# Kernel optimization log

Hardware: AMD Instinct MI355X
Metric: run time of the kernel (lower is better)

The kernel has to match this reference:

```python
import jax, jax.numpy as jnp
import numpy as np

PATCH = 14   # vision_config.patch_size
MERGE = 2    # spatial_merge_size
D = 1024     # vision_config.hidden_size
# pixel (H, W) per image; all dims divisible by PATCH*MERGE = 28
IMAGE_SIZES = np.array([[1540, 1232], [1120, 1540], [896, 1260],
                        [1540, 1540], [1260, 896], [728, 1540]], dtype=np.int64)


def setup_inputs() -> dict:
    key = jax.random.key(0)
    k1, k2 = jax.random.split(key)
    hs = IMAGE_SIZES[:, 0] // PATCH
    ws = IMAGE_SIZES[:, 1] // PATCH
    total_tokens = int(np.sum(hs * ws))  # 47820
    image_features = jax.random.normal(k1, (total_tokens, D), dtype=jnp.float32)
    # nn.Linear(D*MERGE**2 -> D, bias=False): weight [D, D*MERGE**2]
    weight = jax.random.normal(k2, (D, D * MERGE * MERGE), dtype=jnp.float32) * 0.02
    return {"image_features": image_features, "weight": weight,
            "image_sizes": IMAGE_SIZES}


def _merge_patches(image_features, image_sizes):
    """Per-image unfold(kernel=stride=MERGE) -> [n_blocks, D*MERGE^2], concatenated."""
    m = MERGE
    d = image_features.shape[-1]
    sizes = np.asarray(image_sizes)
    hs = sizes[:, 0] // PATCH
    ws = sizes[:, 1] // PATCH
    offsets = np.concatenate([[0], np.cumsum(hs * ws)])
    grids = []
    for i in range(sizes.shape[0]):
        h, w = int(hs[i]), int(ws[i])
        x = jax.lax.dynamic_slice_in_dim(image_features, int(offsets[i]), h * w, 0)
        # [h, w, d] -> blocks of m x m; torch unfold layout is (d, kh, kw) channel-major
        x = x.reshape(h // m, m, w // m, m, d)
        x = x.transpose(0, 2, 4, 1, 3)           # [h/m, w/m, d, m, m]
        x = x.reshape((h // m) * (w // m), d * m * m)
        grids.append(x)
    return jnp.concatenate(grids, axis=0)        # [sum(h*w)/m^2, d*m^2]


def reference(image_features, weight, image_sizes):
    merged = _merge_patches(image_features, image_sizes)
    return merged @ weight.T                     # [N_merged, D]
```

## Files before the change

kernel.cpp:

```cpp
#include <hip/hip_runtime.h>
#include <hip/hip_bf16.h>
#include <stdint.h>

#define K_DIM 4096
#define N_DIM 1024
#define M_TOT 11955

#define BM 128
#define BN 128
#define BK 64
#define NWG_M 94
#define NWG 752

__constant__ int c_wm[6]     = {44, 55, 45, 55, 32, 55};
__constant__ int c_w[6]      = {88, 110, 90, 110, 64, 110};
__constant__ int c_tokoff[6] = {0, 9680, 18480, 24240, 36340, 42100};
__constant__ int c_blkoff[6] = {0, 2420, 4620, 6060, 9085, 10525};

typedef __attribute__((ext_vector_type(8))) short bf16x8;
typedef __attribute__((ext_vector_type(4))) float f32x4;

__global__ __launch_bounds__(256) void wperm_cvt(
    const float* __restrict__ src, __hip_bfloat16* __restrict__ dst)
{
    const int n = blockIdx.x >> 1;
    const int t = (blockIdx.x & 1) * 256 + threadIdx.x;
    const float* row = src + (size_t)n * K_DIM + t * 8;
    float4 a = *(const float4*)row;
    float4 b = *(const float4*)(row + 4);
    const float va[8] = {a.x, a.y, a.z, a.w, b.x, b.y, b.z, b.w};
    __hip_bfloat16* drow = dst + (size_t)n * K_DIM + 2 * t;
#pragma unroll
    for (int seg = 0; seg < 4; ++seg) {
        __hip_bfloat162 h = __float22bfloat162_rn(
            make_float2(va[seg], va[4 + seg]));
        *(__hip_bfloat162*)(drow + seg * 1024) = h;
    }
}

__global__ __launch_bounds__(256) void unfold_cvt(
    const float* __restrict__ feat, __hip_bfloat16* __restrict__ Am)
{
    const int m = blockIdx.x;
    const int t = threadIdx.x;
    const int seg = t >> 6;
    const int d0 = (t & 63) * 16;
    int img = 0;
#pragma unroll
    for (int u = 1; u < 6; ++u) if (m >= c_blkoff[u]) img = u;
    const int bi = m - c_blkoff[img];
    const int wmrg = c_wm[img];
    const int gi = bi / wmrg;
    const int gj = bi - gi * wmrg;
    const int w  = c_w[img];
    const int kh = seg >> 1, kw = seg & 1;
    const int tok = c_tokoff[img] + 2 * gi * w + 2 * gj + kh * w + kw;
    const float4* src = (const float4*)(feat + (size_t)tok * N_DIM + d0);
    float4 v0 = src[0], v1 = src[1], v2 = src[2], v3 = src[3];
    union { __hip_bfloat162 h[8]; uint4 u4[2]; } pk;
    pk.h[0] = __float22bfloat162_rn(make_float2(v0.x, v0.y));
    pk.h[1] = __float22bfloat162_rn(make_float2(v0.z, v0.w));
    pk.h[2] = __float22bfloat162_rn(make_float2(v1.x, v1.y));
    pk.h[3] = __float22bfloat162_rn(make_float2(v1.z, v1.w));
    pk.h[4] = __float22bfloat162_rn(make_float2(v2.x, v2.y));
    pk.h[5] = __float22bfloat162_rn(make_float2(v2.z, v2.w));
    pk.h[6] = __float22bfloat162_rn(make_float2(v3.x, v3.y));
    pk.h[7] = __float22bfloat162_rn(make_float2(v3.z, v3.w));
    uint4* dst = (uint4*)(Am + (size_t)m * K_DIM + seg * 1024 + d0);
    dst[0] = pk.u4[0];
    dst[1] = pk.u4[1];
}

__global__ __launch_bounds__(256) void gemm_bt(
    const __hip_bfloat16* __restrict__ Am,
    const __hip_bfloat16* __restrict__ Wp,
    float* __restrict__ C)
{
    __shared__ __align__(16) __hip_bfloat16 lA[BM * BK];
    __shared__ __align__(16) __hip_bfloat16 lB[BN * BK];

    const int f    = blockIdx.x;
    const int xcd  = f & 7;
    const int slot = f >> 3;
    const int wgid = xcd * NWG_M + slot;
    const int mt   = wgid >> 3;
    const int nt   = wgid & 7;
    const int m0 = mt * BM;
    const int n0 = nt * BN;

    const int tid  = threadIdx.x;
    const int lane = tid & 63;
    const int wave = tid >> 6;
    const int wm = (wave >> 1) * 64;
    const int wn = (wave & 1) * 64;
    const int al = lane & 15;
    const int q  = lane >> 4;
    const int al7 = al & 7;

    const __hip_bfloat16* srcA[4];
    const __hip_bfloat16* srcB[4];
#pragma unroll
    for (int j = 0; j < 4; ++j) {
        const int c = tid + j * 256;
        const int row = c >> 3;
        const int g = (c & 7) ^ (row & 7);
        int gm = m0 + row; if (gm > M_TOT - 1) gm = M_TOT - 1;
        srcA[j] = Am + (size_t)gm * K_DIM + g * 8;
        srcB[j] = Wp + (size_t)(n0 + row) * K_DIM + g * 8;
    }

    f32x4 acc[4][4];
#pragma unroll
    for (int i = 0; i < 4; ++i)
#pragma unroll
        for (int j = 0; j < 4; ++j)
            acc[i][j] = (f32x4){0.f, 0.f, 0.f, 0.f};

    for (int k2 = 0; k2 < K_DIM; k2 += BK) {
#pragma unroll
        for (int j = 0; j < 4; ++j)
            __builtin_amdgcn_global_load_lds(
                (const __attribute__((address_space(1))) void*)(srcA[j] + k2),
                (__attribute__((address_space(3))) void*)(lA + (tid + j * 256) * 8),
                16, 0, 0);
#pragma unroll
        for (int j = 0; j < 4; ++j)
            __builtin_amdgcn_global_load_lds(
                (const __attribute__((address_space(1))) void*)(srcB[j] + k2),
                (__attribute__((address_space(3))) void*)(lB + (tid + j * 256) * 8),
                16, 0, 0);
        __syncthreads();

        bf16x8 af[4], bfr[4];
#pragma unroll
        for (int ks = 0; ks < 2; ++ks) {
#pragma unroll
            for (int mi = 0; mi < 4; ++mi) {
                const int r = wm + mi * 16 + al;
                const int p = (ks * 4 + q) ^ al7;
                af[mi] = *(const bf16x8*)(lA + r * BK + p * 8);
            }
#pragma unroll
            for (int ni = 0; ni < 4; ++ni) {
                const int r = wn + ni * 16 + al;
                const int p = (ks * 4 + q) ^ al7;
                bfr[ni] = *(const bf16x8*)(lB + r * BK + p * 8);
            }
#pragma unroll
            for (int mi = 0; mi < 4; ++mi)
#pragma unroll
                for (int ni = 0; ni < 4; ++ni)
                    acc[mi][ni] = __builtin_amdgcn_mfma_f32_16x16x32_bf16(
                        af[mi], bfr[ni], acc[mi][ni], 0, 0, 0);
        }
        __syncthreads();
    }

#pragma unroll
    for (int mi = 0; mi < 4; ++mi) {
        const int row = m0 + wm + mi * 16 + q * 4;
#pragma unroll
        for (int ni = 0; ni < 4; ++ni) {
            const int col = n0 + wn + ni * 16 + al;
            float* cp = C + (size_t)row * N_DIM + col;
#pragma unroll
            for (int rg = 0; rg < 4; ++rg) {
                if (row + rg < M_TOT) cp[(size_t)rg * N_DIM] = acc[mi][ni][rg];
            }
        }
    }
}

extern "C" void kernel_launch(void* const* d_in, const int* in_sizes, int n_in,
                              void* d_out, int out_size, void* d_ws, size_t ws_size,
                              hipStream_t stream)
{
    const float* feat = (const float*)d_in[0];
    const float* wgt  = (const float*)d_in[1];
    float* out = (float*)d_out;

    __hip_bfloat16* Am = (__hip_bfloat16*)d_ws;
    __hip_bfloat16* wp = (__hip_bfloat16*)((char*)d_ws +
                         (size_t)M_TOT * K_DIM * sizeof(__hip_bfloat16));

    wperm_cvt<<<2048, 256, 0, stream>>>(wgt, wp);
    unfold_cvt<<<M_TOT, 256, 0, stream>>>(feat, Am);
    gemm_bt<<<NWG, 256, 0, stream>>>(Am, wp, out);
}
```

Before: 471.0 us.

## Double-buffer LDS tiles with async global_load_lds prefetch two tiles ahead

Splits the GEMM's LDS A/B tiles into two buffers. Loads for tile k+2 are issued while tile k is computed, and explicit vmcnt waits plus raw barriers replace the per-iteration __syncthreads. This is meant to hide global-memory latency behind the MFMA work, which was previously serialized with loading. The cost is twice the LDS (64KB per block), which may lower occupancy, and it relies on the hand-written vmcnt counts being correct.

```diff
diff --git a/kernel.cpp b/kernel.cpp
--- a/kernel.cpp
+++ b/kernel.cpp
@@ -9,6 +9,7 @@
 #define BM 128
 #define BN 128
 #define BK 64
+#define KT_N 64
 #define NWG_M 94
 #define NWG 752
 
@@ -19,6 +20,11 @@
 
 typedef __attribute__((ext_vector_type(8))) short bf16x8;
 typedef __attribute__((ext_vector_type(4))) float f32x4;
+
+#define BARRIER() do { asm volatile("" ::: "memory"); \
+                       __builtin_amdgcn_s_barrier();  \
+                       asm volatile("" ::: "memory"); } while (0)
+#define WAIT_VM(N) asm volatile("s_waitcnt vmcnt(" #N ")" ::: "memory")
 
 __global__ __launch_bounds__(256) void wperm_cvt(
     const float* __restrict__ src, __hip_bfloat16* __restrict__ dst)
@@ -76,8 +82,8 @@
     const __hip_bfloat16* __restrict__ Wp,
     float* __restrict__ C)
 {
-    __shared__ __align__(16) __hip_bfloat16 lA[BM * BK];
-    __shared__ __align__(16) __hip_bfloat16 lB[BN * BK];
+    __shared__ __align__(16) __hip_bfloat16 lA[2][BM * BK];
+    __shared__ __align__(16) __hip_bfloat16 lB[2][BN * BK];
 
     const int f    = blockIdx.x;
     const int xcd  = f & 7;
@@ -109,6 +115,25 @@
         srcB[j] = Wp + (size_t)(n0 + row) * K_DIM + g * 8;
     }
 
+#define ISSUE_TILE(KT, BUF) do {                                              \
+    const int _off = (KT) * BK;                                               \
+    _Pragma("unroll")                                                         \
+    for (int _j = 0; _j < 4; ++_j)                                            \
+        __builtin_amdgcn_global_load_lds(                                     \
+            (const __attribute__((address_space(1))) void*)(srcA[_j] + _off), \
+            (__attribute__((address_space(3))) void*)(&lA[BUF][0] +           \
+                (tid + _j * 256) * 8), 16, 0, 0);                             \
+    _Pragma("unroll")                                                         \
+    for (int _j = 0; _j < 4; ++_j)                                            \
+        __builtin_amdgcn_global_load_lds(                                     \
+            (const __attribute__((address_space(1))) void*)(srcB[_j] + _off), \
+            (__attribute__((address_space(3))) void*)(&lB[BUF][0] +           \
+                (tid + _j * 256) * 8), 16, 0, 0);                             \
+} while (0)
+
+    ISSUE_TILE(0, 0);
+    ISSUE_TILE(1, 1);
+
     f32x4 acc[4][4];
 #pragma unroll
     for (int i = 0; i < 4; ++i)
@@ -116,21 +141,12 @@
         for (int j = 0; j < 4; ++j)
             acc[i][j] = (f32x4){0.f, 0.f, 0.f, 0.f};
 
-    for (int k2 = 0; k2 < K_DIM; k2 += BK) {
-#pragma unroll
-        for (int j = 0; j < 4; ++j)
-            __builtin_amdgcn_global_load_lds(
-                (const __attribute__((address_space(1))) void*)(srcA[j] + k2),
-                (__attribute__((address_space(3))) void*)(lA + (tid + j * 256) * 8),
-                16, 0, 0);
-#pragma unroll
-        for (int j = 0; j < 4; ++j)
-            __builtin_amdgcn_global_load_lds(
-                (const __attribute__((address_space(1))) void*)(srcB[j] + k2),
-                (__attribute__((address_space(3))) void*)(lB + (tid + j * 256) * 8),
-                16, 0, 0);
-        __syncthreads();
-
+    for (int kt = 0; kt < KT_N; ++kt) {
+        if (kt == KT_N - 1) { WAIT_VM(0); } else { WAIT_VM(8); }
+        BARRIER();
+
+        const __hip_bfloat16* la = &lA[kt & 1][0];
+        const __hip_bfloat16* lb = &lB[kt & 1][0];
         bf16x8 af[4], bfr[4];
 #pragma unroll
         for (int ks = 0; ks < 2; ++ks) {
@@ -138,13 +154,13 @@
             for (int mi = 0; mi < 4; ++mi) {
                 const int r = wm + mi * 16 + al;
                 const int p = (ks * 4 + q) ^ al7;
-                af[mi] = *(const bf16x8*)(lA + r * BK + p * 8);
+                af[mi] = *(const bf16x8*)(la + r * BK + p * 8);
             }
 #pragma unroll
             for (int ni = 0; ni < 4; ++ni) {
                 const int r = wn + ni * 16 + al;
                 const int p = (ks * 4 + q) ^ al7;
-                bfr[ni] = *(const bf16x8*)(lB + r * BK + p * 8);
+                bfr[ni] = *(const bf16x8*)(lb + r * BK + p * 8);
             }
 #pragma unroll
             for (int mi = 0; mi < 4; ++mi)
@@ -153,8 +169,11 @@
                     acc[mi][ni] = __builtin_amdgcn_mfma_f32_16x16x32_bf16(
                         af[mi], bfr[ni], acc[mi][ni], 0, 0, 0);
         }
-        __syncthreads();
-    }
+
+        BARRIER();
+        if (kt + 2 < KT_N) ISSUE_TILE(kt + 2, kt & 1);
+    }
+#undef ISSUE_TILE
 
 #pragma unroll
     for (int mi = 0; mi < 4; ++mi) {
```

New measurement: 456.7 us. -3.0%, faster.
